# Optimization experiments

Measured on AMD Instinct MI355X. Metric: run time of the kernel, lower is better.

The kernel has to match this reference:

```python
import jax, jax.numpy as jnp
import numpy as np

B, T, H, W, D, NH, DEPTH, NCODES = 2, 16, 16, 16, 512, 8, 6, 1024
HW = H * W; DH = D // NH; KH = KW = 3; SIZE = KH * KW; MLP_DIM = 2 * D
NEG = -1e9


def _ln(x, g, b, eps=1e-5):
    m = jnp.mean(x, -1, keepdims=True)
    v = jnp.mean((x - m) ** 2, -1, keepdims=True)
    return (x - m) * jax.lax.rsqrt(v + eps) * g + b


def _rope(x, pos):
    # x: [N, h, T, dh]; half-split rotary embedding
    half = x.shape[-1] // 2
    freqs = 1.0 / (10000.0 ** (jnp.arange(half, dtype=jnp.float32) / half))
    ang = pos[:, None] * freqs[None]            # [T, half]
    cos = jnp.concatenate([jnp.cos(ang), jnp.cos(ang)], -1)
    sin = jnp.concatenate([jnp.sin(ang), jnp.sin(ang)], -1)
    rot = jnp.concatenate([-x[..., half:], x[..., :half]], -1)
    return x * cos + rot * sin


def setup_inputs() -> dict:
    key = jax.random.key(0)
    keys = iter(jax.random.split(key, 64))
    def p(shape, s=0.02):
        return (s * jax.random.normal(next(keys), shape)).astype(jnp.float32)
    inp = dict(
        codes=jax.random.randint(next(keys), (B, T, HW), 0, NCODES),
        emb_table=p((NCODES, D)),
        cls_token=p((1, 1, 1, D)),
        h_emb=p((1, 1, H, D)),
        w_emb=p((1, 1, W, D)),
        emb_norm_g=jnp.ones(D), emb_norm_b=jnp.zeros(D),
        sn_g=jnp.ones((DEPTH, D)), sn_b=jnp.zeros((DEPTH, D)),
        s_wq=p((DEPTH, D, D)), s_bq=jnp.zeros((DEPTH, D)),
        s_wk=p((DEPTH, D, D)), s_bk=jnp.zeros((DEPTH, D)),
        s_wv=p((DEPTH, D, D)), s_bv=jnp.zeros((DEPTH, D)),
        s_wo=p((DEPTH, D, D)), s_bo=jnp.zeros((DEPTH, D)),
        tn_g=jnp.ones((DEPTH, D)), tn_b=jnp.zeros((DEPTH, D)),
        t_wq=p((DEPTH, D, D)), t_bq=jnp.zeros((DEPTH, D)),
        t_wk=p((DEPTH, D, D)), t_bk=jnp.zeros((DEPTH, D)),
        t_wv=p((DEPTH, D, D)), t_bv=jnp.zeros((DEPTH, D)),
        t_wo=p((DEPTH, D, D)), t_bo=jnp.zeros((DEPTH, D)),
        mn_g=jnp.ones((DEPTH, D)), mn_b=jnp.zeros((DEPTH, D)),
        mlp_w1=p((DEPTH, D, MLP_DIM)), mlp_b1=jnp.zeros((DEPTH, MLP_DIM)),
        mlp_w2=p((DEPTH, MLP_DIM, D)), mlp_b2=jnp.zeros((DEPTH, D)),
        fn_g=jnp.ones(D), fn_b=jnp.zeros(D),
    )
    return inp


def reference(codes, emb_table, cls_token, h_emb, w_emb, emb_norm_g, emb_norm_b,
              sn_g, sn_b, s_wq, s_bq, s_wk, s_bk, s_wv, s_bv, s_wo, s_bo,
              tn_g, tn_b, t_wq, t_bq, t_wk, t_bk, t_wv, t_bv, t_wo, t_bo,
              mn_g, mn_b, mlp_w1, mlp_b1, mlp_w2, mlp_b2, fn_g, fn_b):
    T1 = T + 1
    emb = emb_table[codes]                                   # [B,T,HW,D]
    # positional embeddings exactly as torch repeat / repeat_interleave
    x = emb + jnp.tile(h_emb, (1, 1, W, 1)) + jnp.repeat(w_emb, H, axis=2)
    x = jnp.concatenate([x, jnp.broadcast_to(cls_token, (B, 1, HW, D))], axis=1)
    x = _ln(x, emb_norm_g, emb_norm_b)                       # [B,T1,HW,D]

    # temporal causal mask: True = masked
    tmask = jnp.triu(jnp.ones((T1, T1), dtype=bool), 1).at[-1, -1].set(True)
    # spatial out-of-bounds mask [H,W,SIZE] from unfold of ones with zero pad
    ones_pad = jnp.pad(jnp.ones((H, W), jnp.float32), 1)
    smask = jnp.stack([ones_pad[a:a + H, b:b + W]
                       for a in range(KH) for b in range(KW)], -1) == 0

    scale = 1.0 / jnp.sqrt(jnp.float32(DH))
    pos = jnp.arange(T1, dtype=jnp.float32)
    k_list, v_list = [], []
    attn_logits = None
    for i in range(DEPTH):
        # ---- spatial windowed attention on frames 0..T-1 ----
        xg = x[:, :-1].reshape(B, T, H, W, D)
        xn = _ln(xg, sn_g[i], sn_b[i])
        pad = jnp.pad(xn, ((0, 0), (0, 0), (1, 1), (1, 1), (0, 0)))
        nb = jnp.stack([pad[:, :, a:a + H, b:b + W]
                        for a in range(KH) for b in range(KW)], axis=4)  # [B,T,H,W,SIZE,D]
        q = (xn @ s_wq[i] + s_bq[i]).reshape(B, T, H, W, NH, DH)
        kk = (nb @ s_wk[i] + s_bk[i]).reshape(B, T, H, W, SIZE, NH, DH)
        vv = (nb @ s_wv[i] + s_bv[i]).reshape(B, T, H, W, SIZE, NH, DH)
        lg = jnp.einsum('btxynd,btxysnd->btxyns', q, kk) * scale
        lg = jnp.where(smask[None, None, :, :, None, :], NEG, lg)
        a_sp = jax.nn.softmax(lg, -1)
        o = jnp.einsum('btxyns,btxysnd->btxynd', a_sp, vv).reshape(B, T, H, W, D)
        o = o @ s_wo[i] + s_bo[i]
        x_sp = (o + xg).reshape(B, T, HW, D)                 # residual (drop_path=id, eval)
        xt = jnp.concatenate([x_sp, x[:, -1:]], axis=1)      # [B,T1,HW,D]

        # ---- temporal RoPE causal attention over T1 per spatial location ----
        s = xt.transpose(0, 2, 1, 3).reshape(B * HW, T1, D)
        sn_ = _ln(s, tn_g[i], tn_b[i])
        def heads(y):
            return y.reshape(B * HW, T1, NH, DH).transpose(0, 2, 1, 3)
        qt = _rope(heads(sn_ @ t_wq[i] + t_bq[i]), pos)
        kt = _rope(heads(sn_ @ t_wk[i] + t_bk[i]), pos)
        vt = heads(sn_ @ t_wv[i] + t_bv[i])
        lt = jnp.einsum('nhqd,nhkd->nhqk', qt, kt) * scale
        lt = jnp.where(tmask[None, None], NEG, lt)
        at = jax.nn.softmax(lt, -1)
        ot = jnp.einsum('nhqk,nhkd->nhqd', at, vt).transpose(0, 2, 1, 3).reshape(B * HW, T1, D)
        s = (ot @ t_wo[i] + t_bo[i]) + s
        xo = s.reshape(B, HW, T1, D).transpose(0, 2, 1, 3)   # [B,T1,HW,D]
        # average frame 0 over HW and broadcast back (as in torch code)
        xo = xo.at[:, 0].set(jnp.broadcast_to(xo[:, 0].mean(axis=1, keepdims=True), (B, HW, D)))
        attn_logits = lt.reshape(B, HW, NH, T1, T1)

        # ---- MLP (dim -> 2*dim, tanh, -> dim), dropout off in eval ----
        y = jnp.tanh(_ln(xo, mn_g[i], mn_b[i]) @ mlp_w1[i] + mlp_b1[i]) @ mlp_w2[i] + mlp_b2[i]
        x = y + xo
        k_list.append(kt[:, :, :-1, :])
        v_list.append(vt[:, :, :-1, :])

    return _ln(x, fn_g, fn_b), attn_logits, jnp.stack(k_list), jnp.stack(v_list)
```

## Files before the change

kernel.cpp:

```cpp
#include <hip/hip_runtime.h>
#include <hip/hip_bf16.h>
#include <math.h>

#define D_    512
#define NHH   8
#define DH_   64
#define T_    16
#define T1_   17
#define HWL   256
#define B__   2
#define NEGV  -1e9f

typedef __attribute__((ext_vector_type(8))) short short8;
typedef __attribute__((ext_vector_type(4))) short short4v;
typedef __attribute__((ext_vector_type(4))) float f32x4;
typedef __hip_bfloat16 bf16;

__device__ inline float wave_sum(float v){
  #pragma unroll
  for(int o=32;o>0;o>>=1) v += __shfl_xor(v,o,64);
  return v;
}
__device__ inline float b2f(unsigned short s){
  unsigned u = ((unsigned)s)<<16; float f; __builtin_memcpy(&f,&u,4); return f;
}
__device__ inline short f2bs(float f){
  bf16 h = __float2bfloat16(f); short s; __builtin_memcpy(&s,&h,2); return s;
}
__device__ inline void gload_lds16(const void* g, void* l){
  __builtin_amdgcn_global_load_lds((const __attribute__((address_space(1))) void*)g,
                                   (__attribute__((address_space(3))) void*)l, 16, 0, 0);
}

__global__ __launch_bounds__(256) void embed_ln_kernel(
    const int* __restrict__ codes, const float* __restrict__ emb,
    const float* __restrict__ cls, const float* __restrict__ hpos,
    const float* __restrict__ wpos, const float* __restrict__ g,
    const float* __restrict__ bta, bf16* __restrict__ X){
  int row  = blockIdx.x*4 + (threadIdx.x>>6);
  int lane = threadIdx.x & 63;
  int hw = row % HWL; int bt = row / HWL; int t = bt % T1_; int bb = bt / T1_;
  float v[8];
  if(t < T_){
    int code = codes[(bb*T_ + t)*HWL + hw];
    const float4* ep = (const float4*)(emb  + (size_t)code*D_);
    const float4* hp = (const float4*)(hpos + (size_t)(hw & 15)*D_);
    const float4* wp = (const float4*)(wpos + (size_t)(hw >> 4)*D_);
    float4 a0=ep[lane*2], a1=ep[lane*2+1];
    float4 h0=hp[lane*2], h1=hp[lane*2+1];
    float4 w0=wp[lane*2], w1=wp[lane*2+1];
    v[0]=a0.x+h0.x+w0.x; v[1]=a0.y+h0.y+w0.y; v[2]=a0.z+h0.z+w0.z; v[3]=a0.w+h0.w+w0.w;
    v[4]=a1.x+h1.x+w1.x; v[5]=a1.y+h1.y+w1.y; v[6]=a1.z+h1.z+w1.z; v[7]=a1.w+h1.w+w1.w;
  } else {
    const float4* cp = (const float4*)cls;
    float4 c0=cp[lane*2], c1=cp[lane*2+1];
    v[0]=c0.x; v[1]=c0.y; v[2]=c0.z; v[3]=c0.w; v[4]=c1.x; v[5]=c1.y; v[6]=c1.z; v[7]=c1.w;
  }
  float s=0;
  #pragma unroll
  for(int j=0;j<8;j++) s += v[j];
  s = wave_sum(s);
  float mean = s*(1.f/512.f);
  float s2=0;
  #pragma unroll
  for(int j=0;j<8;j++){ float d0=v[j]-mean; s2 += d0*d0; }
  s2 = wave_sum(s2);
  float inv = rsqrtf(s2*(1.f/512.f) + 1e-5f);
  const float4* g4 = (const float4*)g; const float4* b4 = (const float4*)bta;
  float4 gv=g4[lane*2], gw=g4[lane*2+1], bv=b4[lane*2], bw=b4[lane*2+1];
  short4v r0 = { f2bs((v[0]-mean)*inv*gv.x+bv.x), f2bs((v[1]-mean)*inv*gv.y+bv.y),
                 f2bs((v[2]-mean)*inv*gv.z+bv.z), f2bs((v[3]-mean)*inv*gv.w+bv.w) };
  short4v r1 = { f2bs((v[4]-mean)*inv*gw.x+bw.x), f2bs((v[5]-mean)*inv*gw.y+bw.y),
                 f2bs((v[6]-mean)*inv*gw.z+bw.z), f2bs((v[7]-mean)*inv*gw.w+bw.w) };
  bf16* o = X + (size_t)row*D_;
  *(short4v*)&o[lane*8]     = r0;
  *(short4v*)&o[lane*8 + 4] = r1;
}

__global__ __launch_bounds__(256) void ln_kernel(
    const bf16* __restrict__ in, float* __restrict__ out,
    const float* __restrict__ g, const float* __restrict__ bta,
    int c_rpb, int s_rpb){
  int row  = blockIdx.x*4 + (threadIdx.x>>6);
  int lane = threadIdx.x & 63;
  int bb = row / c_rpb; int rem = row - bb*c_rpb;
  short8 vv = *(const short8*)(in + ((size_t)bb*s_rpb + rem)*D_ + lane*8);
  float v[8]; float s=0;
  #pragma unroll
  for(int j=0;j<8;j++){ v[j] = b2f((unsigned short)vv[j]); s += v[j]; }
  s = wave_sum(s);
  float mean = s*(1.f/512.f);
  float s2=0;
  #pragma unroll
  for(int j=0;j<8;j++){ float d0=v[j]-mean; s2 += d0*d0; }
  s2 = wave_sum(s2);
  float inv = rsqrtf(s2*(1.f/512.f) + 1e-5f);
  const float4* g4 = (const float4*)g; const float4* b4 = (const float4*)bta;
  float4 gv=g4[lane*2], gw=g4[lane*2+1], bv=b4[lane*2], bw=b4[lane*2+1];
  float4 o0 = { (v[0]-mean)*inv*gv.x+bv.x, (v[1]-mean)*inv*gv.y+bv.y,
                (v[2]-mean)*inv*gv.z+bv.z, (v[3]-mean)*inv*gv.w+bv.w };
  float4 o1 = { (v[4]-mean)*inv*gw.x+bw.x, (v[5]-mean)*inv*gw.y+bw.y,
                (v[6]-mean)*inv*gw.z+bw.z, (v[7]-mean)*inv*gw.w+bw.w };
  float* o = out + (size_t)row*D_;
  *(float4*)&o[lane*8]     = o0;
  *(float4*)&o[lane*8 + 4] = o1;
}

__global__ __launch_bounds__(256) void ln_bf_kernel(
    const bf16* __restrict__ in, bf16* __restrict__ out,
    const float* __restrict__ g, const float* __restrict__ bta,
    int c_rpb, int s_rpb){
  int row  = blockIdx.x*4 + (threadIdx.x>>6);
  int lane = threadIdx.x & 63;
  int bb = row / c_rpb; int rem = row - bb*c_rpb;
  short8 vv = *(const short8*)(in + ((size_t)bb*s_rpb + rem)*D_ + lane*8);
  float v[8]; float s=0;
  #pragma unroll
  for(int j=0;j<8;j++){ v[j] = b2f((unsigned short)vv[j]); s += v[j]; }
  s = wave_sum(s);
  float mean = s*(1.f/512.f);
  float s2=0;
  #pragma unroll
  for(int j=0;j<8;j++){ float d0=v[j]-mean; s2 += d0*d0; }
  s2 = wave_sum(s2);
  float inv = rsqrtf(s2*(1.f/512.f) + 1e-5f);
  const float4* g4 = (const float4*)g; const float4* b4 = (const float4*)bta;
  float4 gv=g4[lane*2], gw=g4[lane*2+1], bv=b4[lane*2], bw=b4[lane*2+1];
  short4v r0 = { f2bs((v[0]-mean)*inv*gv.x+bv.x), f2bs((v[1]-mean)*inv*gv.y+bv.y),
                 f2bs((v[2]-mean)*inv*gv.z+bv.z), f2bs((v[3]-mean)*inv*gv.w+bv.w) };
  short4v r1 = { f2bs((v[4]-mean)*inv*gw.x+bw.x), f2bs((v[5]-mean)*inv*gw.y+bw.y),
                 f2bs((v[6]-mean)*inv*gw.z+bw.z), f2bs((v[7]-mean)*inv*gw.w+bw.w) };
  bf16* o = out + (size_t)row*D_;
  *(short4v*)&o[lane*8]     = r0;
  *(short4v*)&o[lane*8 + 4] = r1;
}

__global__ __launch_bounds__(256) void wconv_kernel(
    const float* sq, const float* sk, const float* sv, const float* so,
    const float* tq, const float* tk, const float* tv, const float* to,
    const float* w1, const float* w2, bf16* __restrict__ dst){
  __shared__ float sm[32][33];
  int z = blockIdx.z; int i = z/10, id = z - i*10;
  const size_t wo = (size_t)i*262144, mo = (size_t)i*524288;
  bf16* db = dst + (size_t)i*3145728;
  const float* src; bf16* d; int K, N;
  switch(id){
    case 0: src=sq+wo; d=db+0*262144;  K=512;  N=512;  break;
    case 1: src=sk+wo; d=db+1*262144;  K=512;  N=512;  break;
    case 2: src=sv+wo; d=db+2*262144;  K=512;  N=512;  break;
    case 3: src=so+wo; d=db+3*262144;  K=512;  N=512;  break;
    case 4: src=tq+wo; d=db+4*262144;  K=512;  N=512;  break;
    case 5: src=tk+wo; d=db+5*262144;  K=512;  N=512;  break;
    case 6: src=tv+wo; d=db+6*262144;  K=512;  N=512;  break;
    case 7: src=to+wo; d=db+7*262144;  K=512;  N=512;  break;
    case 8: src=w1+mo; d=db+2097152;   K=512;  N=1024; break;
    default:src=w2+mo; d=db+2621440;   K=1024; N=512;  break;
  }
  int n0 = blockIdx.x<<5, k0 = blockIdx.y<<5;
  if(n0 >= N || k0 >= K) return;
  int tx = threadIdx.x & 31, ty = threadIdx.x >> 5;
  #pragma unroll
  for(int j=0;j<4;j++) sm[ty+j*8][tx] = src[(size_t)(k0+ty+j*8)*N + n0+tx];
  __syncthreads();
  #pragma unroll
  for(int j=0;j<4;j++) d[(size_t)(n0+ty+j*8)*K + k0+tx] = __float2bfloat16(sm[tx][ty+j*8]);
}

template<int ACT, bool RES, bool OBF>
__global__ __launch_bounds__(256) void gemm_mfma(
    const bf16* __restrict__ A, const bf16* __restrict__ Wt,
    const float* __restrict__ bias, void* __restrict__ outp,
    const bf16* __restrict__ resid, int K, int N, int c_rpb, int o_rpb){
  __shared__ __align__(16) bf16 As[128*64];
  __shared__ __align__(16) bf16 Bs[128*64];
  const int tid  = threadIdx.x;
  const int lane = tid & 63;
  const int w    = tid >> 6;
  const int row0 = blockIdx.y << 7;
  const int col0 = blockIdx.x << 7;
  const int mb = (w>>1)*64, nb = (w&1)*64;
  size_t ga[4], gb[4];
  #pragma unroll
  for(int r=0;r<4;r++){
    int c = (r*4+w)*64 + lane;
    int rw = c>>3;
    int ks = (c&7) ^ (rw&7);
    ga[r] = (size_t)(row0+rw)*K + (ks<<3);
    gb[r] = (size_t)(col0+rw)*K + (ks<<3);
  }
  f32x4 acc[4][4] = {};
  for(int k0=0;k0<K;k0+=64){
    #pragma unroll
    for(int r=0;r<4;r++){
      gload_lds16(A  + ga[r] + k0, As + (size_t)(r*4+w)*512);
      gload_lds16(Wt + gb[r] + k0, Bs + (size_t)(r*4+w)*512);
    }
    __syncthreads();
    const short8* Av = (const short8*)As;
    const short8* Bv = (const short8*)Bs;
    #pragma unroll
    for(int kk=0;kk<2;kk++){
      const int slot = (lane>>4) + kk*4;
      short8 af[4], bfr[4];
      #pragma unroll
      for(int mi=0;mi<4;mi++){ int rw = mb + mi*16 + (lane&15); af[mi]  = Av[rw*8 + (slot ^ (rw&7))]; }
      #pragma unroll
      for(int ni=0;ni<4;ni++){ int rw = nb + ni*16 + (lane&15); bfr[ni] = Bv[rw*8 + (slot ^ (rw&7))]; }
      #pragma unroll
      for(int mi=0;mi<4;mi++)
        #pragma unroll
        for(int ni=0;ni<4;ni++)
          acc[mi][ni] = __builtin_amdgcn_mfma_f32_16x16x32_bf16(af[mi], bfr[ni], acc[mi][ni], 0,0,0);
    }
    __syncthreads();
  }
  #pragma unroll
  for(int mi=0;mi<4;mi++){
    #pragma unroll
    for(int r=0;r<4;r++){
      int row = row0 + mb + mi*16 + (lane>>4)*4 + r;
      int bb = row / c_rpb;
      size_t orow = (size_t)bb*o_rpb + (row - bb*c_rpb);
      #pragma unroll
      for(int ni=0;ni<4;ni++){
        int col = col0 + nb + ni*16 + (lane&15);
        float v = acc[mi][ni][r] + bias[col];
        if(ACT==1) v = tanhf(v);
        if(RES) v += __bfloat162float(resid[orow*(size_t)N + col]);
        if(OBF) ((bf16*)outp)[orow*(size_t)N + col] = __float2bfloat16(v);
        else    ((float*)outp)[orow*(size_t)N + col] = v;
      }
    }
  }
}

__global__ __launch_bounds__(256) void gemm_mfma64(
    const bf16* __restrict__ A, const bf16* __restrict__ Wt,
    const float* __restrict__ bias, bf16* __restrict__ outp,
    const bf16* __restrict__ resid, int K, int N, int c_rpb, int o_rpb){
  __shared__ __align__(16) bf16 As[2][64*64];
  __shared__ __align__(16) bf16 Bs[2][64*64];
  const int tid  = threadIdx.x;
  const int lane = tid & 63;
  const int w    = tid >> 6;
  const int row0 = blockIdx.y << 6;
  const int col0 = blockIdx.x << 6;
  const int mw = (w>>1)*32, nw = (w&1)*32;
  size_t ga[2], gb[2];
  #pragma unroll
  for(int r=0;r<2;r++){
    int c = (r*4+w)*64 + lane;
    int rw = c>>3;
    int ks = (c&7) ^ (rw&7);
    ga[r] = (size_t)(row0+rw)*K + (ks<<3);
    gb[r] = (size_t)(col0+rw)*K + (ks<<3);
  }
  f32x4 acc[2][2] = {};
  #pragma unroll
  for(int r=0;r<2;r++){
    gload_lds16(A  + ga[r], &As[0][(r*4+w)*512]);
    gload_lds16(Wt + gb[r], &Bs[0][(r*4+w)*512]);
  }
  __syncthreads();
  int cur = 0;
  for(int k0=0;k0<K;k0+=64){
    if(k0+64 < K){
      #pragma unroll
      for(int r=0;r<2;r++){
        gload_lds16(A  + ga[r] + k0+64, &As[cur^1][(r*4+w)*512]);
        gload_lds16(Wt + gb[r] + k0+64, &Bs[cur^1][(r*4+w)*512]);
      }
    }
    const short8* Av = (const short8*)As[cur];
    const short8* Bv = (const short8*)Bs[cur];
    #pragma unroll
    for(int kk=0;kk<2;kk++){
      const int slot = (lane>>4) + kk*4;
      short8 af[2], bfr[2];
      #pragma unroll
      for(int mi=0;mi<2;mi++){ int rw = mw + mi*16 + (lane&15); af[mi]  = Av[rw*8 + (slot ^ (rw&7))]; }
      #pragma unroll
      for(int ni=0;ni<2;ni++){ int rw = nw + ni*16 + (lane&15); bfr[ni] = Bv[rw*8 + (slot ^ (rw&7))]; }
      #pragma unroll
      for(int mi=0;mi<2;mi++)
        #pragma unroll
        for(int ni=0;ni<2;ni++)
          acc[mi][ni] = __builtin_amdgcn_mfma_f32_16x16x32_bf16(af[mi], bfr[ni], acc[mi][ni], 0,0,0);
    }
    __syncthreads();
    cur ^= 1;
  }
  #pragma unroll
  for(int mi=0;mi<2;mi++){
    #pragma unroll
    for(int r=0;r<4;r++){
      int row = row0 + mw + mi*16 + (lane>>4)*4 + r;
      int bb = row / c_rpb;
      size_t orow = (size_t)bb*o_rpb + (row - bb*c_rpb);
      #pragma unroll
      for(int ni=0;ni<2;ni++){
        int col = col0 + nw + ni*16 + (lane&15);
        float v = acc[mi][ni][r] + bias[col];
        v += __bfloat162float(resid[orow*(size_t)N + col]);
        outp[orow*(size_t)N + col] = __float2bfloat16(v);
      }
    }
  }
}

__global__ __launch_bounds__(256) void gemm_qkv(
    const bf16* __restrict__ A, const bf16* __restrict__ Wt,
    const float* __restrict__ bq, const float* __restrict__ bk, const float* __restrict__ bv,
    bf16* __restrict__ Qo, bf16* __restrict__ Ko, bf16* __restrict__ Vo){
  const int K = 512;
  __shared__ __align__(16) bf16 As[128*64];
  __shared__ __align__(16) bf16 Bs[128*64];
  const int tid  = threadIdx.x;
  const int lane = tid & 63;
  const int w    = tid >> 6;
  const int row0 = blockIdx.y << 7;
  const int col0 = blockIdx.x << 7;
  const int mb = (w>>1)*64, nb = (w&1)*64;
  size_t ga[4], gb[4];
  #pragma unroll
  for(int r=0;r<4;r++){
    int c = (r*4+w)*64 + lane;
    int rw = c>>3;
    int ks = (c&7) ^ (rw&7);
    ga[r] = (size_t)(row0+rw)*K + (ks<<3);
    gb[r] = (size_t)(col0+rw)*K + (ks<<3);
  }
  f32x4 acc[4][4] = {};
  for(int k0=0;k0<K;k0+=64){
    #pragma unroll
    for(int r=0;r<4;r++){
      gload_lds16(A  + ga[r] + k0, As + (size_t)(r*4+w)*512);
      gload_lds16(Wt + gb[r] + k0, Bs + (size_t)(r*4+w)*512);
    }
    __syncthreads();
    const short8* Av = (const short8*)As;
    const short8* Bv = (const short8*)Bs;
    #pragma unroll
    for(int kk=0;kk<2;kk++){
      const int slot = (lane>>4) + kk*4;
      short8 af[4], bfr[4];
      #pragma unroll
      for(int mi=0;mi<4;mi++){ int rw = mb + mi*16 + (lane&15); af[mi]  = Av[rw*8 + (slot ^ (rw&7))]; }
      #pragma unroll
      for(int ni=0;ni<4;ni++){ int rw = nb + ni*16 + (lane&15); bfr[ni] = Bv[rw*8 + (slot ^ (rw&7))]; }
      #pragma unroll
      for(int mi=0;mi<4;mi++)
        #pragma unroll
        for(int ni=0;ni<4;ni++)
          acc[mi][ni] = __builtin_amdgcn_mfma_f32_16x16x32_bf16(af[mi], bfr[ni], acc[mi][ni], 0,0,0);
    }
    __syncthreads();
  }
  const int sel = col0 >> 9;
  bf16* outp = (sel==0) ? Qo : (sel==1 ? Ko : Vo);
  const float* bp = (sel==0) ? bq : (sel==1 ? bk : bv);
  const int cb = col0 & 511;
  #pragma unroll
  for(int mi=0;mi<4;mi++){
    #pragma unroll
    for(int r=0;r<4;r++){
      int row = row0 + mb + mi*16 + (lane>>4)*4 + r;
      #pragma unroll
      for(int ni=0;ni<4;ni++){
        int col = cb + nb + ni*16 + (lane&15);
        outp[(size_t)row*512 + col] = __float2bfloat16(acc[mi][ni][r] + bp[col]);
      }
    }
  }
}

__global__ __launch_bounds__(256) void spatial_attn_kernel(
    const bf16* __restrict__ Q, const bf16* __restrict__ K,
    const bf16* __restrict__ V, bf16* __restrict__ O){
  int loc = blockIdx.x;
  int hw = loc & 255;
  int hh = hw >> 4, ww = hw & 15;
  int tid = threadIdx.x, lane = tid & 63, w = tid >> 6;
  int h = w*2 + (lane>>5);
  int j = lane & 31;
  size_t base = (size_t)loc*D_ + h*DH_ + 2*j;
  unsigned uq = *(const unsigned*)&Q[base];
  float q0 = b2f((unsigned short)uq), q1 = b2f((unsigned short)(uq>>16));
  float lg[9]; int nrow[9];
  #pragma unroll
  for(int s=0;s<9;s++){
    int a = s/3 - 1, b2_ = s%3 - 1;
    int nh = hh + a, nw = ww + b2_;
    bool ok = ((unsigned)nh < 16u) && ((unsigned)nw < 16u);
    nrow[s] = ok ? (loc - hw + (nh<<4) + nw) : -1;
    float p = 0.f;
    if(ok){
      unsigned uk = *(const unsigned*)&K[(size_t)nrow[s]*D_ + h*DH_ + 2*j];
      p = q0*b2f((unsigned short)uk) + q1*b2f((unsigned short)(uk>>16));
    }
    #pragma unroll
    for(int o=16;o>0;o>>=1) p += __shfl_xor(p, o, 64);
    lg[s] = ok ? p*0.125f : NEGV;
  }
  float m = lg[0];
  #pragma unroll
  for(int s=1;s<9;s++) m = fmaxf(m, lg[s]);
  float den = 0.f, wv[9];
  #pragma unroll
  for(int s=0;s<9;s++){ wv[s] = __expf(lg[s]-m); den += wv[s]; }
  float inv = 1.f/den;
  float a0 = 0.f, a1 = 0.f;
  #pragma unroll
  for(int s=0;s<9;s++){
    if(nrow[s] >= 0){
      unsigned uv = *(const unsigned*)&V[(size_t)nrow[s]*D_ + h*DH_ + 2*j];
      a0 += wv[s]*b2f((unsigned short)uv);
      a1 += wv[s]*b2f((unsigned short)(uv>>16));
    }
  }
  unsigned up = (unsigned)(unsigned short)f2bs(a0*inv) | ((unsigned)(unsigned short)f2bs(a1*inv) << 16);
  *(unsigned*)&O[base] = up;
}

__global__ __launch_bounds__(512) void fused_tattn(
    const bf16* __restrict__ Qb, const bf16* __restrict__ Kb, const bf16* __restrict__ Vb,
    bf16* __restrict__ O, float* __restrict__ kout, float* __restrict__ vout,
    float* __restrict__ ltout, int write_lt){
  __shared__ __align__(16) bf16 Qs[17*520];
  __shared__ __align__(16) bf16 Ks[17*520];
  __shared__ __align__(16) bf16 Vs[17*512];
  __shared__ float Ws[8][17][18];
  const int tid = threadIdx.x, w = tid>>6, lane = tid&63;
  const int hw = blockIdx.x & 255, b = blockIdx.x >> 8;
  const size_t tstr = (size_t)HWL*D_;
  const size_t rb0 = ((size_t)(b*T1_)*HWL + hw)*D_;
  for(int t=w; t<17; t+=8){
    size_t src = rb0 + (size_t)t*tstr + lane*8;
    *(short8*)&Qs[t*520 + lane*8] = *(const short8*)&Qb[src];
    *(short8*)&Ks[t*520 + lane*8] = *(const short8*)&Kb[src];
    *(short8*)&Vs[t*512 + lane*8] = *(const short8*)&Vb[src];
  }
  __syncthreads();
  {
    int i = lane & 31;
    float freq = __expf(-9.210340372f * (float)i * (1.f/32.f));
    bf16* P = (lane < 32) ? Qs : Ks;
    #pragma unroll
    for(int t=0;t<17;t++){
      float sn, cs; __sincosf((float)t*freq, &sn, &cs);
      int idx = t*520 + w*64 + i;
      float x1 = __bfloat162float(P[idx]);
      float x2 = __bfloat162float(P[idx+32]);
      P[idx]    = __float2bfloat16(x1*cs - x2*sn);
      P[idx+32] = __float2bfloat16(x2*cs + x1*sn);
    }
  }
  __syncthreads();
  {
    size_t eb = (((size_t)(b*HWL + hw)*NHH + w)*16)*64 + lane;
    #pragma unroll
    for(int t=0;t<16;t++){
      kout[eb + t*64] = __bfloat162float(Ks[t*520 + w*64 + lane]);
      vout[eb + t*64] = __bfloat162float(Vs[t*512 + w*64 + lane]);
    }
  }
  size_t lb = ((size_t)(b*HWL + hw)*NHH + w)*289;
  for(int p=lane; p<289; p+=64){
    int t = p/17, u = p - t*17;
    float d = 0.f;
    #pragma unroll
    for(int jj=0;jj<8;jj++){
      short8 qq = *(short8*)&Qs[t*520 + w*64 + jj*8];
      short8 kk = *(short8*)&Ks[u*520 + w*64 + jj*8];
      #pragma unroll
      for(int e=0;e<8;e++) d += b2f((unsigned short)qq[e]) * b2f((unsigned short)kk[e]);
    }
    bool masked = (u > t) || (t == 16 && u == 16);
    float lg = masked ? NEGV : d*0.125f;
    Ws[w][t][u] = lg;
    if(write_lt) ltout[lb + t*17 + u] = lg;
  }
  __syncthreads();
  if(lane < 17){
    float m = -1e30f;
    #pragma unroll
    for(int u=0;u<17;u++) m = fmaxf(m, Ws[w][lane][u]);
    float den = 0.f, e[17];
    #pragma unroll
    for(int u=0;u<17;u++){ e[u] = __expf(Ws[w][lane][u]-m); den += e[u]; }
    float inv = 1.f/den;
    #pragma unroll
    for(int u=0;u<17;u++) Ws[w][lane][u] = e[u]*inv;
  }
  __syncthreads();
  float Vr[17];
  #pragma unroll
  for(int u=0;u<17;u++) Vr[u] = __bfloat162float(Vs[u*512 + w*64 + lane]);
  #pragma unroll
  for(int t=0;t<17;t++){
    float acc = 0.f;
    #pragma unroll
    for(int u=0;u<17;u++) acc += Ws[w][t][u]*Vr[u];
    O[rb0 + (size_t)t*tstr + w*64 + lane] = __float2bfloat16(acc);
  }
}

__global__ __launch_bounds__(256) void avg_frame0_kernel(bf16* __restrict__ X){
  int d = blockIdx.x & 511; int bb = blockIdx.x >> 9;
  int hw = threadIdx.x;
  __shared__ float sm[256];
  size_t idx = ((size_t)(bb*T1_)*HWL + hw)*D_ + d;
  sm[hw] = __bfloat162float(X[idx]);
  __syncthreads();
  for(int o=128;o>0;o>>=1){ if(hw<o) sm[hw] += sm[hw+o]; __syncthreads(); }
  X[idx] = __float2bfloat16(sm[0]*(1.f/256.f));
}

extern "C" void kernel_launch(void* const* d_in, const int* in_sizes, int n_in,
                              void* d_out, int out_size, void* d_ws, size_t ws_size,
                              hipStream_t stream){
  const int*   codes = (const int*)  d_in[0];
  const float* emb   = (const float*)d_in[1];
  const float* cls   = (const float*)d_in[2];
  const float* hpos  = (const float*)d_in[3];
  const float* wpos  = (const float*)d_in[4];
  const float* eng   = (const float*)d_in[5];
  const float* enb   = (const float*)d_in[6];
  const float* sn_g  = (const float*)d_in[7];
  const float* sn_b  = (const float*)d_in[8];
  const float* s_wq  = (const float*)d_in[9];
  const float* s_bq  = (const float*)d_in[10];
  const float* s_wk  = (const float*)d_in[11];
  const float* s_bk  = (const float*)d_in[12];
  const float* s_wv  = (const float*)d_in[13];
  const float* s_bv  = (const float*)d_in[14];
  const float* s_wo  = (const float*)d_in[15];
  const float* s_bo  = (const float*)d_in[16];
  const float* tn_g  = (const float*)d_in[17];
  const float* tn_b  = (const float*)d_in[18];
  const float* t_wq  = (const float*)d_in[19];
  const float* t_bq  = (const float*)d_in[20];
  const float* t_wk  = (const float*)d_in[21];
  const float* t_bk  = (const float*)d_in[22];
  const float* t_wv  = (const float*)d_in[23];
  const float* t_bv  = (const float*)d_in[24];
  const float* t_wo  = (const float*)d_in[25];
  const float* t_bo  = (const float*)d_in[26];
  const float* mn_g  = (const float*)d_in[27];
  const float* mn_b  = (const float*)d_in[28];
  const float* mw1   = (const float*)d_in[29];
  const float* mb1   = (const float*)d_in[30];
  const float* mw2   = (const float*)d_in[31];
  const float* mb2   = (const float*)d_in[32];
  const float* fn_g  = (const float*)d_in[33];
  const float* fn_b  = (const float*)d_in[34];

  const size_t NX = 4456448;
  bf16* Xb  = (bf16*)d_ws;
  bf16* XNb = Xb  + NX;
  bf16* Qb  = XNb + NX;
  bf16* Kb  = Qb  + NX;
  bf16* Vb  = Kb  + NX;
  bf16* Wt  = Vb  + NX;
  bf16* HIDb= Qb;

  float* out0 = (float*)d_out;
  float* out1 = out0 + NX;
  float* out2 = out1 + 1183744;
  float* out3 = out2 + 25165824;

  const int RS = B__*T_*HWL;
  const int RT = B__*T1_*HWL;
  dim3 gQs(12, 64);
  dim3 gQt(12, 68);
  dim3 g64s(8, 128);
  dim3 g64t(8, 136);
  dim3 gM1(8, 68);
  dim3 wcg(32, 32, 60);

  embed_ln_kernel<<<RT/4, 256, 0, stream>>>(codes, emb, cls, hpos, wpos, eng, enb, Xb);
  wconv_kernel<<<wcg,256,0,stream>>>(s_wq, s_wk, s_wv, s_wo, t_wq, t_wk, t_wv, t_wo, mw1, mw2, Wt);

  for(int i=0;i<6;i++){
    bf16* Wl = Wt + (size_t)i*3145728;
    ln_bf_kernel<<<RS/4,256,0,stream>>>(Xb, XNb, sn_g+i*D_, sn_b+i*D_, T_*HWL, T1_*HWL);
    gemm_qkv<<<gQs,256,0,stream>>>(XNb, Wl, s_bq+i*D_, s_bk+i*D_, s_bv+i*D_, Qb, Kb, Vb);
    spatial_attn_kernel<<<RS,256,0,stream>>>(Qb, Kb, Vb, XNb);
    gemm_mfma64<<<g64s,256,0,stream>>>(XNb, Wl+3*262144, s_bo+i*D_, Xb, Xb, 512, 512, T_*HWL, T1_*HWL);
    ln_bf_kernel<<<RT/4,256,0,stream>>>(Xb, XNb, tn_g+i*D_, tn_b+i*D_, T1_*HWL, T1_*HWL);
    gemm_qkv<<<gQt,256,0,stream>>>(XNb, Wl+4*262144, t_bq+i*D_, t_bk+i*D_, t_bv+i*D_, Qb, Kb, Vb);
    fused_tattn<<<512,512,0,stream>>>(Qb, Kb, Vb, XNb,
                                      out2+(size_t)i*4194304, out3+(size_t)i*4194304,
                                      out1, (i==5)?1:0);
    gemm_mfma64<<<g64t,256,0,stream>>>(XNb, Wl+7*262144, t_bo+i*D_, Xb, Xb, 512, 512, RT, RT);
    avg_frame0_kernel<<<1024,256,0,stream>>>(Xb);
    ln_bf_kernel<<<RT/4,256,0,stream>>>(Xb, XNb, mn_g+i*D_, mn_b+i*D_, T1_*HWL, T1_*HWL);
    gemm_mfma<1,false,true ><<<gM1,256,0,stream>>>(XNb, Wl+2097152, mb1+i*1024, HIDb, nullptr, 512, 1024, RT, RT);
    gemm_mfma64<<<g64t,256,0,stream>>>(HIDb, Wl+2621440, mb2+i*D_, Xb, Xb, 1024, 512, RT, RT);
  }
  ln_kernel<<<RT/4,256,0,stream>>>(Xb, out0, fn_g, fn_b, T1_*HWL, T1_*HWL);
}
```

Measured before the change: 1.363 ms.

## Fold LayerNorm into following GEMMs via row stats and precomputed gamma/beta terms

```diff
diff --git a/kernel.cpp b/kernel.cpp
--- a/kernel.cpp
+++ b/kernel.cpp
@@ -77,6 +77,29 @@
   *(short4v*)&o[lane*8 + 4] = r1;
 }
 
+__global__ __launch_bounds__(256) void stats_kernel(
+    const bf16* __restrict__ in, float* __restrict__ MU, float* __restrict__ SI,
+    int c_rpb, int s_rpb){
+  int row  = blockIdx.x*4 + (threadIdx.x>>6);
+  int lane = threadIdx.x & 63;
+  int bb = row / c_rpb;
+  size_t xrow = (size_t)bb*s_rpb + (row - bb*c_rpb);
+  short8 vv = *(const short8*)(in + xrow*D_ + lane*8);
+  float v[8]; float s=0;
+  #pragma unroll
+  for(int j=0;j<8;j++){ v[j] = b2f((unsigned short)vv[j]); s += v[j]; }
+  s = wave_sum(s);
+  float mean = s*(1.f/512.f);
+  float s2=0;
+  #pragma unroll
+  for(int j=0;j<8;j++){ float d0=v[j]-mean; s2 += d0*d0; }
+  s2 = wave_sum(s2);
+  if(lane == 0){
+    MU[row] = mean;
+    SI[row] = rsqrtf(s2*(1.f/512.f) + 1e-5f);
+  }
+}
+
 __global__ __launch_bounds__(256) void ln_kernel(
     const bf16* __restrict__ in, float* __restrict__ out,
     const float* __restrict__ g, const float* __restrict__ bta,
@@ -106,54 +129,26 @@
   *(float4*)&o[lane*8 + 4] = o1;
 }
 
-__global__ __launch_bounds__(256) void ln_bf_kernel(
-    const bf16* __restrict__ in, bf16* __restrict__ out,
-    const float* __restrict__ g, const float* __restrict__ bta,
-    int c_rpb, int s_rpb){
-  int row  = blockIdx.x*4 + (threadIdx.x>>6);
-  int lane = threadIdx.x & 63;
-  int bb = row / c_rpb; int rem = row - bb*c_rpb;
-  short8 vv = *(const short8*)(in + ((size_t)bb*s_rpb + rem)*D_ + lane*8);
-  float v[8]; float s=0;
-  #pragma unroll
-  for(int j=0;j<8;j++){ v[j] = b2f((unsigned short)vv[j]); s += v[j]; }
-  s = wave_sum(s);
-  float mean = s*(1.f/512.f);
-  float s2=0;
-  #pragma unroll
-  for(int j=0;j<8;j++){ float d0=v[j]-mean; s2 += d0*d0; }
-  s2 = wave_sum(s2);
-  float inv = rsqrtf(s2*(1.f/512.f) + 1e-5f);
-  const float4* g4 = (const float4*)g; const float4* b4 = (const float4*)bta;
-  float4 gv=g4[lane*2], gw=g4[lane*2+1], bv=b4[lane*2], bw=b4[lane*2+1];
-  short4v r0 = { f2bs((v[0]-mean)*inv*gv.x+bv.x), f2bs((v[1]-mean)*inv*gv.y+bv.y),
-                 f2bs((v[2]-mean)*inv*gv.z+bv.z), f2bs((v[3]-mean)*inv*gv.w+bv.w) };
-  short4v r1 = { f2bs((v[4]-mean)*inv*gw.x+bw.x), f2bs((v[5]-mean)*inv*gw.y+bw.y),
-                 f2bs((v[6]-mean)*inv*gw.z+bw.z), f2bs((v[7]-mean)*inv*gw.w+bw.w) };
-  bf16* o = out + (size_t)row*D_;
-  *(short4v*)&o[lane*8]     = r0;
-  *(short4v*)&o[lane*8 + 4] = r1;
-}
-
 __global__ __launch_bounds__(256) void wconv_kernel(
     const float* sq, const float* sk, const float* sv, const float* so,
     const float* tq, const float* tk, const float* tv, const float* to,
-    const float* w1, const float* w2, bf16* __restrict__ dst){
+    const float* w1, const float* w2,
+    const float* sng, const float* tng, const float* mng, bf16* __restrict__ dst){
   __shared__ float sm[32][33];
   int z = blockIdx.z; int i = z/10, id = z - i*10;
   const size_t wo = (size_t)i*262144, mo = (size_t)i*524288;
   bf16* db = dst + (size_t)i*3145728;
-  const float* src; bf16* d; int K, N;
+  const float* src; bf16* d; int K, N; const float* g = nullptr;
   switch(id){
-    case 0: src=sq+wo; d=db+0*262144;  K=512;  N=512;  break;
-    case 1: src=sk+wo; d=db+1*262144;  K=512;  N=512;  break;
-    case 2: src=sv+wo; d=db+2*262144;  K=512;  N=512;  break;
+    case 0: src=sq+wo; d=db+0*262144;  K=512;  N=512;  g=sng+i*512; break;
+    case 1: src=sk+wo; d=db+1*262144;  K=512;  N=512;  g=sng+i*512; break;
+    case 2: src=sv+wo; d=db+2*262144;  K=512;  N=512;  g=sng+i*512; break;
     case 3: src=so+wo; d=db+3*262144;  K=512;  N=512;  break;
-    case 4: src=tq+wo; d=db+4*262144;  K=512;  N=512;  break;
-    case 5: src=tk+wo; d=db+5*262144;  K=512;  N=512;  break;
-    case 6: src=tv+wo; d=db+6*262144;  K=512;  N=512;  break;
+    case 4: src=tq+wo; d=db+4*262144;  K=512;  N=512;  g=tng+i*512; break;
+    case 5: src=tk+wo; d=db+5*262144;  K=512;  N=512;  g=tng+i*512; break;
+    case 6: src=tv+wo; d=db+6*262144;  K=512;  N=512;  g=tng+i*512; break;
     case 7: src=to+wo; d=db+7*262144;  K=512;  N=512;  break;
-    case 8: src=w1+mo; d=db+2097152;   K=512;  N=1024; break;
+    case 8: src=w1+mo; d=db+2097152;   K=512;  N=1024; g=mng+i*512; break;
     default:src=w2+mo; d=db+2621440;   K=1024; N=512;  break;
   }
   int n0 = blockIdx.x<<5, k0 = blockIdx.y<<5;
@@ -162,15 +157,48 @@
   #pragma unroll
   for(int j=0;j<4;j++) sm[ty+j*8][tx] = src[(size_t)(k0+ty+j*8)*N + n0+tx];
   __syncthreads();
-  #pragma unroll
-  for(int j=0;j<4;j++) d[(size_t)(n0+ty+j*8)*K + k0+tx] = __float2bfloat16(sm[tx][ty+j*8]);
-}
-
-template<int ACT, bool RES, bool OBF>
-__global__ __launch_bounds__(256) void gemm_mfma(
+  float gk = g ? g[k0+tx] : 1.0f;
+  #pragma unroll
+  for(int j=0;j<4;j++) d[(size_t)(n0+ty+j*8)*K + k0+tx] = __float2bfloat16(sm[tx][ty+j*8]*gk);
+}
+
+__global__ __launch_bounds__(256) void gcb_kernel(
+    const float* sq, const float* sk, const float* sv,
+    const float* tq, const float* tk, const float* tv, const float* w1,
+    const float* sng, const float* snb, const float* tng, const float* tnb,
+    const float* mng, const float* mnb,
+    const float* sbq, const float* sbk, const float* sbv,
+    const float* tbq, const float* tbk, const float* tbv, const float* mb1,
+    float* __restrict__ G, float* __restrict__ CB){
+  int z = blockIdx.x; int i = z/16; int rem = z - i*16;
+  int mat, chunk;
+  if(rem < 12){ mat = rem>>1; chunk = rem&1; } else { mat = 6; chunk = rem-12; }
+  const float* W; const float* g; const float* b; const float* bias; int N; int obase;
+  switch(mat){
+    case 0: W=sq+(size_t)i*262144; g=sng+i*512; b=snb+i*512; bias=sbq+i*512; N=512; obase=i*4096+0;    break;
+    case 1: W=sk+(size_t)i*262144; g=sng+i*512; b=snb+i*512; bias=sbk+i*512; N=512; obase=i*4096+512;  break;
+    case 2: W=sv+(size_t)i*262144; g=sng+i*512; b=snb+i*512; bias=sbv+i*512; N=512; obase=i*4096+1024; break;
+    case 3: W=tq+(size_t)i*262144; g=tng+i*512; b=tnb+i*512; bias=tbq+i*512; N=512; obase=i*4096+1536; break;
+    case 4: W=tk+(size_t)i*262144; g=tng+i*512; b=tnb+i*512; bias=tbk+i*512; N=512; obase=i*4096+2048; break;
+    case 5: W=tv+(size_t)i*262144; g=tng+i*512; b=tnb+i*512; bias=tbv+i*512; N=512; obase=i*4096+2560; break;
+    default:W=w1+(size_t)i*524288; g=mng+i*512; b=mnb+i*512; bias=mb1+i*1024;N=1024;obase=i*4096+3072; break;
+  }
+  int cn = chunk*256 + threadIdx.x;
+  float ag = 0.f, ab = 0.f;
+  for(int k=0;k<512;k++){
+    float w = W[(size_t)k*N + cn];
+    ag += g[k]*w; ab += b[k]*w;
+  }
+  G [obase + cn] = ag;
+  CB[obase + cn] = ab + bias[cn];
+}
+
+__global__ __launch_bounds__(256) void gemm_mlp1(
     const bf16* __restrict__ A, const bf16* __restrict__ Wt,
-    const float* __restrict__ bias, void* __restrict__ outp,
-    const bf16* __restrict__ resid, int K, int N, int c_rpb, int o_rpb){
+    const float* __restrict__ MU, const float* __restrict__ SI,
+    const float* __restrict__ G, const float* __restrict__ CB,
+    bf16* __restrict__ outp){
+  const int K = 512, N = 1024;
   __shared__ __align__(16) bf16 As[128*64];
   __shared__ __align__(16) bf16 Bs[128*64];
   const int tid  = threadIdx.x;
@@ -219,16 +247,12 @@
     #pragma unroll
     for(int r=0;r<4;r++){
       int row = row0 + mb + mi*16 + (lane>>4)*4 + r;
-      int bb = row / c_rpb;
-      size_t orow = (size_t)bb*o_rpb + (row - bb*c_rpb);
+      float mu = MU[row], si = SI[row];
       #pragma unroll
       for(int ni=0;ni<4;ni++){
         int col = col0 + nb + ni*16 + (lane&15);
-        float v = acc[mi][ni][r] + bias[col];
-        if(ACT==1) v = tanhf(v);
-        if(RES) v += __bfloat162float(resid[orow*(size_t)N + col]);
-        if(OBF) ((bf16*)outp)[orow*(size_t)N + col] = __float2bfloat16(v);
-        else    ((float*)outp)[orow*(size_t)N + col] = v;
+        float v = si*(acc[mi][ni][r] - mu*G[col]) + CB[col];
+        outp[(size_t)row*N + col] = __float2bfloat16(tanhf(v));
       }
     }
   }
@@ -310,8 +334,10 @@
 
 __global__ __launch_bounds__(256) void gemm_qkv(
     const bf16* __restrict__ A, const bf16* __restrict__ Wt,
-    const float* __restrict__ bq, const float* __restrict__ bk, const float* __restrict__ bv,
-    bf16* __restrict__ Qo, bf16* __restrict__ Ko, bf16* __restrict__ Vo){
+    const float* __restrict__ MU, const float* __restrict__ SI,
+    const float* __restrict__ G, const float* __restrict__ CB,
+    bf16* __restrict__ Qo, bf16* __restrict__ Ko, bf16* __restrict__ Vo,
+    int c_rpb, int s_rpb){
   const int K = 512;
   __shared__ __align__(16) bf16 As[128*64];
   __shared__ __align__(16) bf16 Bs[128*64];
@@ -321,13 +347,15 @@
   const int row0 = blockIdx.y << 7;
   const int col0 = blockIdx.x << 7;
   const int mb = (w>>1)*64, nb = (w&1)*64;
+  const int bb0 = row0 / c_rpb;
+  const size_t xbase = (size_t)bb0*s_rpb + (row0 - bb0*c_rpb);
   size_t ga[4], gb[4];
   #pragma unroll
   for(int r=0;r<4;r++){
     int c = (r*4+w)*64 + lane;
     int rw = c>>3;
     int ks = (c&7) ^ (rw&7);
-    ga[r] = (size_t)(row0+rw)*K + (ks<<3);
+    ga[r] = (xbase+rw)*K + (ks<<3);
     gb[r] = (size_t)(col0+rw)*K + (ks<<3);
   }
   f32x4 acc[4][4] = {};
@@ -358,17 +386,19 @@
   }
   const int sel = col0 >> 9;
   bf16* outp = (sel==0) ? Qo : (sel==1 ? Ko : Vo);
-  const float* bp = (sel==0) ? bq : (sel==1 ? bk : bv);
-  const int cb = col0 & 511;
+  const int cb512 = col0 & 511;
   #pragma unroll
   for(int mi=0;mi<4;mi++){
     #pragma unroll
     for(int r=0;r<4;r++){
       int row = row0 + mb + mi*16 + (lane>>4)*4 + r;
+      float mu = MU[row], si = SI[row];
       #pragma unroll
       for(int ni=0;ni<4;ni++){
-        int col = cb + nb + ni*16 + (lane&15);
-        outp[(size_t)row*512 + col] = __float2bfloat16(acc[mi][ni][r] + bp[col]);
+        int col = col0 + nb + ni*16 + (lane&15);
+        float v = si*(acc[mi][ni][r] - mu*G[col]) + CB[col];
+        int oc = cb512 + nb + ni*16 + (lane&15);
+        outp[(size_t)row*512 + oc] = __float2bfloat16(v);
       }
     }
   }
@@ -506,14 +536,17 @@
 }
 
 __global__ __launch_bounds__(256) void avg_frame0_kernel(bf16* __restrict__ X){
-  int d = blockIdx.x & 511; int bb = blockIdx.x >> 9;
-  int hw = threadIdx.x;
-  __shared__ float sm[256];
-  size_t idx = ((size_t)(bb*T1_)*HWL + hw)*D_ + d;
-  sm[hw] = __bfloat162float(X[idx]);
+  int b = blockIdx.x >> 3, c = blockIdx.x & 7;
+  int ro = threadIdx.x >> 6, dd = threadIdx.x & 63;
+  size_t base = ((size_t)(b*T1_)*HWL)*D_ + c*64 + dd;
+  float acc = 0.f;
+  for(int r=ro; r<256; r+=4) acc += __bfloat162float(X[base + (size_t)r*D_]);
+  __shared__ float sm[4][64];
+  sm[ro][dd] = acc;
   __syncthreads();
-  for(int o=128;o>0;o>>=1){ if(hw<o) sm[hw] += sm[hw+o]; __syncthreads(); }
-  X[idx] = __float2bfloat16(sm[0]*(1.f/256.f));
+  float v = (sm[0][dd]+sm[1][dd]+sm[2][dd]+sm[3][dd])*(1.f/256.f);
+  bf16 bv = __float2bfloat16(v);
+  for(int r=ro; r<256; r+=4) X[base + (size_t)r*D_] = bv;
 }
 
 extern "C" void kernel_launch(void* const* d_in, const int* in_sizes, int n_in,
@@ -562,6 +595,10 @@
   bf16* Kb  = Qb  + NX;
   bf16* Vb  = Kb  + NX;
   bf16* Wt  = Vb  + NX;
+  float* MU = (float*)(Wt + 6*3145728);
+  float* SI = MU + 8704;
+  float* Gb = SI + 8704;
+  float* CBb= Gb + 24576;
   bf16* HIDb= Qb;
 
   float* out0 = (float*)d_out;
@@ -579,23 +616,28 @@
   dim3 wcg(32, 32, 60);
 
   embed_ln_kernel<<<RT/4, 256, 0, stream>>>(codes, emb, cls, hpos, wpos, eng, enb, Xb);
-  wconv_kernel<<<wcg,256,0,stream>>>(s_wq, s_wk, s_wv, s_wo, t_wq, t_wk, t_wv, t_wo, mw1, mw2, Wt);
+  wconv_kernel<<<wcg,256,0,stream>>>(s_wq, s_wk, s_wv, s_wo, t_wq, t_wk, t_wv, t_wo,
+                                     mw1, mw2, sn_g, tn_g, mn_g, Wt);
+  gcb_kernel<<<96,256,0,stream>>>(s_wq, s_wk, s_wv, t_wq, t_wk, t_wv, mw1,
+                                  sn_g, sn_b, tn_g, tn_b, mn_g, mn_b,
+                                  s_bq, s_bk, s_bv, t_bq, t_bk, t_bv, mb1, Gb, CBb);
 
   for(int i=0;i<6;i++){
     bf16* Wl = Wt + (size_t)i*3145728;
-    ln_bf_kernel<<<RS/4,256,0,stream>>>(Xb, XNb, sn_g+i*D_, sn_b+i*D_, T_*HWL, T1_*HWL);
-    gemm_qkv<<<gQs,256,0,stream>>>(XNb, Wl, s_bq+i*D_, s_bk+i*D_, s_bv+i*D_, Qb, Kb, Vb);
+    float* Gi = Gb + i*4096; float* Ci = CBb + i*4096;
+    stats_kernel<<<RS/4,256,0,stream>>>(Xb, MU, SI, T_*HWL, T1_*HWL);
+    gemm_qkv<<<gQs,256,0,stream>>>(Xb, Wl, MU, SI, Gi, Ci, Qb, Kb, Vb, T_*HWL, T1_*HWL);
     spatial_attn_kernel<<<RS,256,0,stream>>>(Qb, Kb, Vb, XNb);
     gemm_mfma64<<<g64s,256,0,stream>>>(XNb, Wl+3*262144, s_bo+i*D_, Xb, Xb, 512, 512, T_*HWL, T1_*HWL);
-    ln_bf_kernel<<<RT/4,256,0,stream>>>(Xb, XNb, tn_g+i*D_, tn_b+i*D_, T1_*HWL, T1_*HWL);
-    gemm_qkv<<<gQt,256,0,stream>>>(XNb, Wl+4*262144, t_bq+i*D_, t_bk+i*D_, t_bv+i*D_, Qb, Kb, Vb);
+    stats_kernel<<<RT/4,256,0,stream>>>(Xb, MU, SI, RT, RT);
+    gemm_qkv<<<gQt,256,0,stream>>>(Xb, Wl+4*262144, MU, SI, Gi+1536, Ci+1536, Qb, Kb, Vb, RT, RT);
     fused_tattn<<<512,512,0,stream>>>(Qb, Kb, Vb, XNb,
                                       out2+(size_t)i*4194304, out3+(size_t)i*4194304,
                                       out1, (i==5)?1:0);
     gemm_mfma64<<<g64t,256,0,stream>>>(XNb, Wl+7*262144, t_bo+i*D_, Xb, Xb, 512, 512, RT, RT);
-    avg_frame0_kernel<<<1024,256,0,stream>>>(Xb);
-    ln_bf_kernel<<<RT/4,256,0,stream>>>(Xb, XNb, mn_g+i*D_, mn_b+i*D_, T1_*HWL, T1_*HWL);
-    gemm_mfma<1,false,true ><<<gM1,256,0,stream>>>(XNb, Wl+2097152, mb1+i*1024, HIDb, nullptr, 512, 1024, RT, RT);
+    avg_frame0_kernel<<<16,256,0,stream>>>(Xb);
+    stats_kernel<<<RT/4,256,0,stream>>>(Xb, MU, SI, RT, RT);
+    gemm_mlp1<<<gM1,256,0,stream>>>(Xb, Wl+2097152, MU, SI, Gi+3072, Ci+3072, HIDb);
     gemm_mfma64<<<g64t,256,0,stream>>>(HIDb, Wl+2621440, mb2+i*D_, Xb, Xb, 1024, 512, RT, RT);
   }
   ln_kernel<<<RT/4,256,0,stream>>>(Xb, out0, fn_g, fn_b, T1_*HWL, T1_*HWL);
```

New measurement: 1.459 ms. 1.07x slower.
